# Performance work log

Hardware: AMD Instinct MI355X
Metric: run time of the kernel (lower is better)

Reference implementation:

```python
import jax, jax.numpy as jnp
import numpy as np

N = 100000   # nodes
E = 800000   # edges
H = 64       # hidden_channels (also input feature dim via lazy Linear)
OUT = 2      # out_channels
G = 64       # graphs in batch
EPS = 1e-5   # BatchNorm eps
N_PRE, N_CONV, N_POST = 3, 6, 3


def setup_inputs() -> dict:
    key = jax.random.key(0)
    ks = jax.random.split(key, 20)
    s = 0.1
    inp = {
        "x": jax.random.normal(ks[0], (N, H), jnp.float32),
        "edge_index": jax.random.randint(ks[1], (2, E), 0, N, dtype=jnp.int64),
        "batch": jnp.sort(jax.random.randint(ks[2], (N,), 0, G, dtype=jnp.int64)),
        # pre-processing MLP + BN params
        "pre_W": jax.random.normal(ks[3], (N_PRE, H, H), jnp.float32) * s,
        "pre_b": jax.random.normal(ks[4], (N_PRE, H), jnp.float32) * s,
        "pre_g": jnp.ones((N_PRE, H), jnp.float32),
        "pre_beta": jnp.zeros((N_PRE, H), jnp.float32),
        # GCNConv params (weight + bias per layer)
        "conv_W": jax.random.normal(ks[5], (N_CONV, H, H), jnp.float32) * s,
        "conv_b": jax.random.normal(ks[6], (N_CONV, H), jnp.float32) * s,
        # post-processing MLP + BN params
        "post_W": jax.random.normal(ks[7], (N_POST, H, H), jnp.float32) * s,
        "post_b": jax.random.normal(ks[8], (N_POST, H), jnp.float32) * s,
        "post_g": jnp.ones((N_POST, H), jnp.float32),
        "post_beta": jnp.zeros((N_POST, H), jnp.float32),
        # final head: H->H, H->H, H->OUT
        "fin_W0": jax.random.normal(ks[9], (H, H), jnp.float32) * s,
        "fin_b0": jax.random.normal(ks[10], (H,), jnp.float32) * s,
        "fin_W1": jax.random.normal(ks[11], (H, H), jnp.float32) * s,
        "fin_b1": jax.random.normal(ks[12], (H,), jnp.float32) * s,
        "fin_W2": jax.random.normal(ks[13], (H, OUT), jnp.float32) * s,
        "fin_b2": jax.random.normal(ks[14], (OUT,), jnp.float32) * s,
    }
    return inp


def _bn(h, g, b):
    # BatchNorm1d, training mode: biased batch statistics over node dim
    m = h.mean(0)
    v = h.var(0)
    return (h - m) * jax.lax.rsqrt(v + EPS) * g + b


def _gcn(h, src, dst, dinv, W, b):
    # PyG GCNConv: h' = D^-1/2 (A+I) D^-1/2 (h W) + b, sum-aggregated at dst
    hw = h @ W                                   # [N,H]
    norm = dinv[src] * dinv[dst]                 # [E]
    agg = jax.ops.segment_sum(hw[src] * norm[:, None], dst, num_segments=N)
    agg = agg + hw * (dinv * dinv)[:, None]      # self-loop contribution
    return agg + b


def reference(x, edge_index, batch, pre_W, pre_b, pre_g, pre_beta,
              conv_W, conv_b, post_W, post_b, post_g, post_beta,
              fin_W0, fin_b0, fin_W1, fin_b1, fin_W2, fin_b2):
    src, dst = edge_index[0], edge_index[1]
    # gcn_norm degree with self-loops (in-degree at dst), edge_weight = 1
    deg = jax.ops.segment_sum(jnp.ones((E,), x.dtype), dst, num_segments=N) + 1.0
    dinv = jax.lax.rsqrt(deg)

    h = x
    # pre-processing: Linear -> BN, relu except last
    for i in range(N_PRE):
        h = _bn(h @ pre_W[i] + pre_b[i], pre_g[i], pre_beta[i])
        if i != N_PRE - 1:
            h = jax.nn.relu(h)
    # GCNConv stack with residual adds
    for i in range(N_CONV):
        h = _gcn(h, src, dst, dinv, conv_W[i], conv_b[i]) + h
        if i != N_CONV - 1:
            h = jax.nn.relu(h)
    # post-processing: Linear -> BN, relu except last
    for i in range(N_POST):
        h = _bn(h @ post_W[i] + post_b[i], post_g[i], post_beta[i])
        if i != N_POST - 1:
            h = jax.nn.relu(h)
    # global_mean_pool over graphs
    counts = jax.ops.segment_sum(jnp.ones((N,), h.dtype), batch, num_segments=G)
    pooled = jax.ops.segment_sum(h, batch, num_segments=G) / jnp.maximum(counts, 1.0)[:, None]
    # final head (dropout is identity in eval)
    z = jax.nn.relu(pooled @ fin_W0 + fin_b0)
    z = jax.nn.relu(z @ fin_W1 + fin_b1)
    return z @ fin_W2 + fin_b2
```

## Files before the change

kernel.cpp:

```cpp
#include <hip/hip_runtime.h>

#define N_NODES 100000
#define N_EDGES 800000
#define HID 64
#define NGRAPH 64
#define OUTC 2
#define BN_EPS 1e-5f
#define GEMM_BLK ((N_NODES + 63) / 64)
#define POOL_SUB 16
#define BSHIFT 11
#define NBUCK 64
#define NBUCK_ACT ((N_NODES + (1 << BSHIFT) - 1) >> BSHIFT)
#define NEB_BLK ((N_EDGES + 2047) / 2048)

typedef __attribute__((ext_vector_type(8))) short bf16x8;
typedef __attribute__((ext_vector_type(4))) float f32x4;
typedef __attribute__((ext_vector_type(2))) float f32x2;

__device__ __forceinline__ unsigned short f2bf(float f) {
    unsigned int u = __float_as_uint(f);
    u = (u + 0x7FFFu + ((u >> 16) & 1u)) >> 16;
    return (unsigned short)u;
}
__device__ __forceinline__ float bflo(unsigned int u) { return __uint_as_float(u << 16); }
__device__ __forceinline__ float bfhi(unsigned int u) { return __uint_as_float(u & 0xFFFF0000u); }
__device__ __forceinline__ unsigned int bfpack(float a, float b) {
    return (unsigned int)f2bf(a) | ((unsigned int)f2bf(b) << 16);
}
__device__ __forceinline__ f32x2 bfpair(unsigned int w) {
    f32x2 p;
    p.x = __uint_as_float(w << 16);
    p.y = __uint_as_float(w & 0xFFFF0000u);
    return p;
}
__device__ __forceinline__ f32x2 pk_add(f32x2 a, f32x2 b) {
    f32x2 d;
    asm("v_pk_add_f32 %0, %1, %2" : "=v"(d) : "v"(a), "v"(b));
    return d;
}

template <int IN_MODE, bool IN_FP32, bool ADD_BIAS, bool ROW_SCALE, bool STATS>
__global__ __launch_bounds__(256) void k_gemm(const void* __restrict__ Xv,
                                              const float* __restrict__ W,
                                              const float* __restrict__ bias,
                                              const float* __restrict__ dinv,
                                              const float* __restrict__ scsh,
                                              unsigned short* __restrict__ Y,
                                              float* __restrict__ partial, int n) {
    __shared__ __align__(16) unsigned short sXb[64][72];
    __shared__ __align__(16) unsigned short sWT[64][72];
    __shared__ float sDinv[64];
    const int tid  = threadIdx.x;
    const int row0 = blockIdx.x * 64;

    #pragma unroll
    for (int i = tid; i < 1024; i += 256) {
        int k = i >> 4, c4 = (i & 15) << 2;
        float4 w = *reinterpret_cast<const float4*>(&W[k * 64 + c4]);
        sWT[c4 + 0][k] = f2bf(w.x);
        sWT[c4 + 1][k] = f2bf(w.y);
        sWT[c4 + 2][k] = f2bf(w.z);
        sWT[c4 + 3][k] = f2bf(w.w);
    }
    if (IN_FP32) {
        const float* X = (const float*)Xv;
        #pragma unroll
        for (int f = tid; f < 1024; f += 256) {
            int r = f >> 4, c4 = (f & 15) << 2;
            float4 v = make_float4(0.f, 0.f, 0.f, 0.f);
            if (row0 + r < n)
                v = *reinterpret_cast<const float4*>(&X[(size_t)(row0 + r) * HID + c4]);
            if (IN_MODE >= 1) {
                float4 sc = *reinterpret_cast<const float4*>(&scsh[c4]);
                float4 sh = *reinterpret_cast<const float4*>(&scsh[64 + c4]);
                v.x = v.x * sc.x + sh.x; v.y = v.y * sc.y + sh.y;
                v.z = v.z * sc.z + sh.z; v.w = v.w * sc.w + sh.w;
                if (IN_MODE == 2) {
                    v.x = fmaxf(v.x, 0.f); v.y = fmaxf(v.y, 0.f);
                    v.z = fmaxf(v.z, 0.f); v.w = fmaxf(v.w, 0.f);
                }
            }
            sXb[r][c4 + 0] = f2bf(v.x);
            sXb[r][c4 + 1] = f2bf(v.y);
            sXb[r][c4 + 2] = f2bf(v.z);
            sXb[r][c4 + 3] = f2bf(v.w);
        }
    } else {
        const unsigned short* X = (const unsigned short*)Xv;
        #pragma unroll
        for (int f = tid; f < 512; f += 256) {
            int r = f >> 3, c8 = (f & 7) << 3;
            uint4 u = make_uint4(0u, 0u, 0u, 0u);
            if (row0 + r < n)
                u = *reinterpret_cast<const uint4*>(&X[(size_t)(row0 + r) * HID + c8]);
            if (IN_MODE >= 1) {
                float v[8];
                v[0] = bflo(u.x); v[1] = bfhi(u.x);
                v[2] = bflo(u.y); v[3] = bfhi(u.y);
                v[4] = bflo(u.z); v[5] = bfhi(u.z);
                v[6] = bflo(u.w); v[7] = bfhi(u.w);
                #pragma unroll
                for (int k = 0; k < 8; ++k) {
                    v[k] = v[k] * scsh[c8 + k] + scsh[64 + c8 + k];
                    if (IN_MODE == 2) v[k] = fmaxf(v[k], 0.f);
                }
                u.x = bfpack(v[0], v[1]); u.y = bfpack(v[2], v[3]);
                u.z = bfpack(v[4], v[5]); u.w = bfpack(v[6], v[7]);
            }
            *reinterpret_cast<uint4*>(&sXb[r][c8]) = u;
        }
    }
    if (ROW_SCALE && tid < 64)
        sDinv[tid] = (row0 + tid < n) ? dinv[row0 + tid] : 0.f;
    __syncthreads();

    const int lane = tid & 63;
    const int wv   = tid >> 6;
    const int cl   = lane & 15;
    const int kg   = lane >> 4;
    const int col  = (wv << 4) + cl;

    const f32x4 zero = {0.f, 0.f, 0.f, 0.f};
    f32x4 acc[4];
    #pragma unroll
    for (int m = 0; m < 4; ++m) acc[m] = zero;

    #pragma unroll
    for (int k0 = 0; k0 < 64; k0 += 32) {
        bf16x8 bfrag = *reinterpret_cast<const bf16x8*>(&sWT[col][k0 + (kg << 3)]);
        #pragma unroll
        for (int m = 0; m < 4; ++m) {
            bf16x8 afrag = *reinterpret_cast<const bf16x8*>(&sXb[(m << 4) + cl][k0 + (kg << 3)]);
            acc[m] = __builtin_amdgcn_mfma_f32_16x16x32_bf16(afrag, bfrag, acc[m], 0, 0, 0);
        }
    }

    const float bb = ADD_BIAS ? bias[col] : 0.f;
    float colS = 0.f, colQ = 0.f;
    #pragma unroll
    for (int m = 0; m < 4; ++m) {
        #pragma unroll
        for (int j = 0; j < 4; ++j) {
            int rl = (m << 4) + (kg << 2) + j;
            int r  = row0 + rl;
            if (r < n) {
                float s = ROW_SCALE ? sDinv[rl] : 1.f;
                float o = acc[m][j] * s + bb;
                Y[(size_t)r * HID + col] = f2bf(o);
                if (STATS) { colS += o; colQ += o * o; }
            }
        }
    }
    if (STATS) {
        colS += __shfl_xor(colS, 16); colQ += __shfl_xor(colQ, 16);
        colS += __shfl_xor(colS, 32); colQ += __shfl_xor(colQ, 32);
        if (kg == 0) {
            partial[blockIdx.x * 128 + col]      = colS;
            partial[blockIdx.x * 128 + 64 + col] = colQ;
        }
    }
}

__global__ __launch_bounds__(256) void k_statsfin(const float* __restrict__ partial,
                                                  const float* __restrict__ g,
                                                  const float* __restrict__ beta,
                                                  float* __restrict__ scsh, int n) {
    int c = blockIdx.x, t = threadIdx.x;
    float S = 0.f, Q = 0.f;
    for (int b = t; b < GEMM_BLK; b += 256) {
        S += partial[b * 128 + c];
        Q += partial[b * 128 + 64 + c];
    }
    __shared__ float ss[256], sq[256];
    ss[t] = S; sq[t] = Q;
    __syncthreads();
    for (int off = 128; off > 0; off >>= 1) {
        if (t < off) { ss[t] += ss[t + off]; sq[t] += sq[t + off]; }
        __syncthreads();
    }
    if (t == 0) {
        float nf = (float)n;
        float m  = ss[0] / nf;
        float v  = sq[0] / nf - m * m;
        float sc = rsqrtf(v + BN_EPS) * g[c];
        scsh[c]      = sc;
        scsh[64 + c] = beta[c] - m * sc;
    }
}

__global__ __launch_bounds__(256) void k_hist(const int* __restrict__ dst,
                                              int* __restrict__ histmat) {
    __shared__ int lh[NBUCK];
    int t = threadIdx.x;
    if (t < NBUCK) lh[t] = 0;
    __syncthreads();
    int base = blockIdx.x * 2048;
    for (int i = t; i < 2048; i += 256) {
        int e = base + i;
        if (e < N_EDGES) atomicAdd(&lh[dst[e] >> BSHIFT], 1);
    }
    __syncthreads();
    if (t < NBUCK) histmat[blockIdx.x * NBUCK + t] = lh[t];
}

__global__ __launch_bounds__(256) void k_escan(const int* __restrict__ histmat,
                                               int* __restrict__ blockoff,
                                               int* __restrict__ bucketbase) {
    __shared__ int csum[4][NBUCK];
    __shared__ int cbase[4][NBUCK];
    __shared__ int tot[NBUCK + 1];
    int t = threadIdx.x;
    int b = t & 63, c = t >> 6;
    const int CHUNK = (NEB_BLK + 3) / 4;
    int lo = c * CHUNK, hi = min(lo + CHUNK, NEB_BLK);
    int s = 0;
    #pragma unroll 8
    for (int blk = lo; blk < hi; ++blk) s += histmat[blk * NBUCK + b];
    csum[c][b] = s;
    __syncthreads();
    if (t < NBUCK) {
        int r = 0;
        #pragma unroll
        for (int c2 = 0; c2 < 4; ++c2) { cbase[c2][t] = r; r += csum[c2][t]; }
        tot[t] = r;
    }
    __syncthreads();
    if (t == 0) {
        int r = 0;
        for (int b2 = 0; b2 < NBUCK; ++b2) { int v = tot[b2]; tot[b2] = r; r += v; }
        tot[NBUCK] = r;
    }
    __syncthreads();
    if (t <= NBUCK) bucketbase[t] = tot[t];
    int r = cbase[c][b];
    #pragma unroll 8
    for (int blk = lo; blk < hi; ++blk) {
        blockoff[blk * NBUCK + b] = r;
        r += histmat[blk * NBUCK + b];
    }
}

__global__ __launch_bounds__(256) void k_reorder(const int* __restrict__ src,
                                                 const int* __restrict__ dst,
                                                 const int* __restrict__ blockoff,
                                                 const int* __restrict__ bucketbase,
                                                 int2* __restrict__ esort) {
    __shared__ int lcur[NBUCK];
    int t = threadIdx.x;
    if (t < NBUCK) lcur[t] = 0;
    __syncthreads();
    int base = blockIdx.x * 2048;
    for (int i = t; i < 2048; i += 256) {
        int e = base + i;
        if (e < N_EDGES) {
            int d = dst[e];
            int b = d >> BSHIFT;
            int r = atomicAdd(&lcur[b], 1);
            esort[bucketbase[b] + blockoff[blockIdx.x * NBUCK + b] + r] =
                make_int2(src[e], d);
        }
    }
}

__global__ __launch_bounds__(256) void k_csr(const int2* __restrict__ esort,
                                             const int* __restrict__ bucketbase,
                                             int* __restrict__ rowptr,
                                             int* __restrict__ colidx,
                                             float* __restrict__ dinv,
                                             float* __restrict__ rdinv) {
    __shared__ int lh[1 << BSHIFT];
    __shared__ int ctot[256];
    int t = threadIdx.x;
    int b = blockIdx.x;
    int node0 = b << BSHIFT;
    int nNodes = min(1 << BSHIFT, N_NODES - node0);
    int e0 = bucketbase[b], e1 = bucketbase[b + 1];
    #pragma unroll
    for (int i = t; i < (1 << BSHIFT); i += 256) lh[i] = 0;
    __syncthreads();
    for (int e = e0 + t; e < e1; e += 256)
        atomicAdd(&lh[esort[e].y - node0], 1);
    __syncthreads();
    int c0 = t * 8;
    int cnt[8];
    int s = 0;
    #pragma unroll
    for (int j = 0; j < 8; ++j) { cnt[j] = lh[c0 + j]; s += cnt[j]; }
    ctot[t] = s;
    __syncthreads();
    int v = ctot[t];
    for (int off = 1; off < 256; off <<= 1) {
        int x = (t >= off) ? ctot[t - off] : 0;
        __syncthreads();
        ctot[t] += x;
        __syncthreads();
    }
    int run = ctot[t] - v;
    #pragma unroll
    for (int j = 0; j < 8; ++j) {
        int idx = c0 + j;
        int cv = cnt[j];
        lh[idx] = run;
        if (idx < nNodes) {
            rowptr[node0 + idx] = e0 + run;
            float dg = (float)cv + 1.f;
            dinv[node0 + idx]  = rsqrtf(dg);
            rdinv[node0 + idx] = sqrtf(dg);
        }
        run += cv;
    }
    __syncthreads();
    for (int e = e0 + t; e < e1; e += 256) {
        int2 ed = esort[e];
        int r = atomicAdd(&lh[ed.y - node0], 1);
        colidx[e0 + r] = ed.x;
    }
    if (b == 0 && t == 0) rowptr[N_NODES] = N_EDGES;
}

__global__ __launch_bounds__(256) void k_mkg(const unsigned short* __restrict__ H,
                                             const float* __restrict__ scsh,
                                             const float* __restrict__ dinv,
                                             unsigned short* __restrict__ G) {
    int i = blockIdx.x * 256 + threadIdx.x;
    if (i >= N_NODES * 8) return;
    int row = i >> 3, c8 = (i & 7) << 3;
    uint4 u = *reinterpret_cast<const uint4*>(&H[(size_t)row * HID + c8]);
    float di = dinv[row];
    float v[8];
    v[0] = bflo(u.x); v[1] = bfhi(u.x);
    v[2] = bflo(u.y); v[3] = bfhi(u.y);
    v[4] = bflo(u.z); v[5] = bfhi(u.z);
    v[6] = bflo(u.w); v[7] = bfhi(u.w);
    #pragma unroll
    for (int k = 0; k < 8; ++k)
        v[k] = (v[k] * scsh[c8 + k] + scsh[64 + c8 + k]) * di;
    uint4 o;
    o.x = bfpack(v[0], v[1]); o.y = bfpack(v[2], v[3]);
    o.z = bfpack(v[4], v[5]); o.w = bfpack(v[6], v[7]);
    *reinterpret_cast<uint4*>(&G[(size_t)row * HID + c8]) = o;
}

template <bool LAST>
__global__ __launch_bounds__(1024) void k_conv(const int* __restrict__ rowptr,
                                               const int* __restrict__ colidx,
                                               const unsigned short* __restrict__ G,
                                               const float* __restrict__ dinv,
                                               const float* __restrict__ rdinv,
                                               const float* __restrict__ W,
                                               const float* __restrict__ bias,
                                               unsigned short* __restrict__ OutT) {
    __shared__ __align__(16) unsigned short sXb[64][72];
    __shared__ __align__(16) unsigned short sG[64][72];
    __shared__ __align__(16) unsigned short sWT[64][72];
    __shared__ float red[16][8][64];
    __shared__ float sDinv[64], sRD[64];
    const int tid   = threadIdx.x;
    const int node0 = blockIdx.x * 64;

    {
        int k = tid >> 4, c4 = (tid & 15) << 2;
        float4 w = *reinterpret_cast<const float4*>(&W[k * 64 + c4]);
        sWT[c4 + 0][k] = f2bf(w.x);
        sWT[c4 + 1][k] = f2bf(w.y);
        sWT[c4 + 2][k] = f2bf(w.z);
        sWT[c4 + 3][k] = f2bf(w.w);
    }
    if (tid < 64) {
        int nd = node0 + tid;
        sDinv[tid] = (nd < N_NODES) ? dinv[nd] : 0.f;
        sRD[tid]   = (nd < N_NODES) ? rdinv[nd] : 0.f;
    }

    const int wv   = tid >> 6;
    const int lane = tid & 63;
    const int slot = lane >> 3;
    const int c8   = (lane & 7) << 3;

    #pragma unroll 1
    for (int it = 0; it < 4; ++it) {
        const int dl = (wv << 2) + it;
        const int d  = node0 + dl;
        const bool valid = d < N_NODES;

        f32x2 a0 = {0.f, 0.f}, a1 = {0.f, 0.f}, a2 = {0.f, 0.f}, a3 = {0.f, 0.f};
        if (valid) {
            if (slot == 7) {
                uint4 v = *reinterpret_cast<const uint4*>(&G[(size_t)d * HID + c8]);
                a0 = pk_add(a0, bfpair(v.x));
                a1 = pk_add(a1, bfpair(v.y));
                a2 = pk_add(a2, bfpair(v.z));
                a3 = pk_add(a3, bfpair(v.w));
            }
            const int j0 = rowptr[d], j1 = rowptr[d + 1];
            for (int j = j0 + slot; j < j1; j += 8) {
                int s = colidx[j];
                uint4 v = *reinterpret_cast<const uint4*>(&G[(size_t)s * HID + c8]);
                a0 = pk_add(a0, bfpair(v.x));
                a1 = pk_add(a1, bfpair(v.y));
                a2 = pk_add(a2, bfpair(v.z));
                a3 = pk_add(a3, bfpair(v.w));
            }
        }
        *reinterpret_cast<float4*>(&red[wv][slot][c8])     = make_float4(a0.x, a0.y, a1.x, a1.y);
        *reinterpret_cast<float4*>(&red[wv][slot][c8 + 4]) = make_float4(a2.x, a2.y, a3.x, a3.y);
        __builtin_amdgcn_wave_barrier();
        float s = 0.f;
        #pragma unroll
        for (int t2 = 0; t2 < 8; ++t2) s += red[wv][t2][lane];

        if (valid) {
            float z = s * sDinv[dl];
            sXb[dl][lane] = f2bf(z);
            sG[dl][lane]  = G[(size_t)d * HID + lane];
        } else {
            sXb[dl][lane] = 0;
            sG[dl][lane]  = 0;
        }
    }
    __syncthreads();

    const int rt = wv & 3, ct = wv >> 2;
    const int cl = lane & 15, kg = lane >> 4;
    const int col = (ct << 4) + cl;

    f32x4 acc = {0.f, 0.f, 0.f, 0.f};
    #pragma unroll
    for (int k0 = 0; k0 < 64; k0 += 32) {
        bf16x8 bfrag = *reinterpret_cast<const bf16x8*>(&sWT[col][k0 + (kg << 3)]);
        bf16x8 afrag = *reinterpret_cast<const bf16x8*>(&sXb[(rt << 4) + cl][k0 + (kg << 3)]);
        acc = __builtin_amdgcn_mfma_f32_16x16x32_bf16(afrag, bfrag, acc, 0, 0, 0);
    }

    const float bb = bias[col];
    #pragma unroll
    for (int j = 0; j < 4; ++j) {
        int rl = (rt << 4) + (kg << 2) + j;
        int r  = node0 + rl;
        if (r < N_NODES) {
            float h = bflo((unsigned int)sG[rl][col]) * sRD[rl];
            float o = acc[j] + bb + h;
            if (!LAST) {
                o = fmaxf(o, 0.f);
                o *= sDinv[rl];
            }
            OutT[(size_t)r * HID + col] = f2bf(o);
        }
    }
}

__device__ __forceinline__ int lowerb(const int* __restrict__ b, int n, int v) {
    int lo = 0, hi = n;
    while (lo < hi) { int m = (lo + hi) >> 1; if (b[m] < v) lo = m + 1; else hi = m; }
    return lo;
}

__global__ __launch_bounds__(256) void k_pool1(const unsigned short* __restrict__ Y,
                                               const int* __restrict__ batch,
                                               float* __restrict__ partial2) {
    int g  = blockIdx.x >> 4;
    int sb = blockIdx.x & 15;
    int tid = threadIdx.x, col = tid & 63, rg = tid >> 6;
    int lo = lowerb(batch, N_NODES, g);
    int hi = lowerb(batch, N_NODES, g + 1);
    int cnt = hi - lo;
    int st = lo + (int)(((long long)cnt * sb) >> 4);
    int en = lo + (int)(((long long)cnt * (sb + 1)) >> 4);
    float s = 0.f;
    for (int r = st + rg; r < en; r += 4)
        s += bflo((unsigned int)Y[(size_t)r * HID + col]);
    __shared__ float ls[4][64];
    ls[rg][col] = s;
    __syncthreads();
    if (tid < 64)
        partial2[(size_t)blockIdx.x * 64 + tid] =
            ls[0][tid] + ls[1][tid] + ls[2][tid] + ls[3][tid];
}

__global__ __launch_bounds__(256) void k_final(const float* __restrict__ partial2,
                                               const int* __restrict__ batch,
                                               const float* __restrict__ scsh,
                                               const float* __restrict__ W0,
                                               const float* __restrict__ b0,
                                               const float* __restrict__ W1,
                                               const float* __restrict__ b1,
                                               const float* __restrict__ W2,
                                               const float* __restrict__ b2,
                                               float* __restrict__ out) {
    __shared__ float sA[64][68];
    __shared__ float sC[64][68];
    __shared__ float sW[64][64];
    __shared__ int sOff[NGRAPH + 1];
    const int tid = threadIdx.x;
    const int tr = tid >> 4, tc = tid & 15;

    if (tid <= NGRAPH) sOff[tid] = lowerb(batch, N_NODES, tid);
    {
        const float4* w = reinterpret_cast<const float4*>(W0);
        float4* s = reinterpret_cast<float4*>(&sW[0][0]);
        #pragma unroll
        for (int i = tid; i < 1024; i += 256) s[i] = w[i];
    }
    __syncthreads();

    for (int i = tid; i < NGRAPH * HID; i += 256) {
        int g = i >> 6, c = i & 63;
        float S = 0.f;
        #pragma unroll
        for (int sb = 0; sb < POOL_SUB; ++sb)
            S += partial2[(size_t)(g * POOL_SUB + sb) * 64 + c];
        int cnt = sOff[g + 1] - sOff[g];
        float v = 0.f;
        if (cnt > 0) v = (S / (float)cnt) * scsh[c] + scsh[64 + c];
        sA[g][c] = v;
    }
    __syncthreads();

    {
        float4 acc[4];
        #pragma unroll
        for (int i = 0; i < 4; ++i) acc[i] = make_float4(0.f, 0.f, 0.f, 0.f);
        #pragma unroll 16
        for (int k = 0; k < 64; ++k) {
            const float4 bv = *reinterpret_cast<const float4*>(&sW[k][tc << 2]);
            float a[4];
            #pragma unroll
            for (int i = 0; i < 4; ++i) a[i] = sA[(tr << 2) + i][k];
            #pragma unroll
            for (int i = 0; i < 4; ++i) {
                acc[i].x += a[i] * bv.x; acc[i].y += a[i] * bv.y;
                acc[i].z += a[i] * bv.z; acc[i].w += a[i] * bv.w;
            }
        }
        float4 bb = *reinterpret_cast<const float4*>(&b0[tc << 2]);
        #pragma unroll
        for (int i = 0; i < 4; ++i) {
            float4 o;
            o.x = fmaxf(acc[i].x + bb.x, 0.f);
            o.y = fmaxf(acc[i].y + bb.y, 0.f);
            o.z = fmaxf(acc[i].z + bb.z, 0.f);
            o.w = fmaxf(acc[i].w + bb.w, 0.f);
            *reinterpret_cast<float4*>(&sC[(tr << 2) + i][tc << 2]) = o;
        }
    }
    __syncthreads();
    {
        const float4* w = reinterpret_cast<const float4*>(W1);
        float4* s = reinterpret_cast<float4*>(&sW[0][0]);
        #pragma unroll
        for (int i = tid; i < 1024; i += 256) s[i] = w[i];
    }
    __syncthreads();
    {
        float4 acc[4];
        #pragma unroll
        for (int i = 0; i < 4; ++i) acc[i] = make_float4(0.f, 0.f, 0.f, 0.f);
        #pragma unroll 16
        for (int k = 0; k < 64; ++k) {
            const float4 bv = *reinterpret_cast<const float4*>(&sW[k][tc << 2]);
            float a[4];
            #pragma unroll
            for (int i = 0; i < 4; ++i) a[i] = sC[(tr << 2) + i][k];
            #pragma unroll
            for (int i = 0; i < 4; ++i) {
                acc[i].x += a[i] * bv.x; acc[i].y += a[i] * bv.y;
                acc[i].z += a[i] * bv.z; acc[i].w += a[i] * bv.w;
            }
        }
        float4 bb = *reinterpret_cast<const float4*>(&b1[tc << 2]);
        #pragma unroll
        for (int i = 0; i < 4; ++i) {
            float4 o;
            o.x = fmaxf(acc[i].x + bb.x, 0.f);
            o.y = fmaxf(acc[i].y + bb.y, 0.f);
            o.z = fmaxf(acc[i].z + bb.z, 0.f);
            o.w = fmaxf(acc[i].w + bb.w, 0.f);
            *reinterpret_cast<float4*>(&sA[(tr << 2) + i][tc << 2]) = o;
        }
    }
    __syncthreads();

    if (tid < NGRAPH * OUTC) {
        int r = tid >> 1, c = tid & 1;
        float acc = b2[c];
        #pragma unroll 8
        for (int k = 0; k < 64; ++k) acc += sA[r][k] * W2[k * OUTC + c];
        out[tid] = acc;
    }
}

extern "C" void kernel_launch(void* const* d_in, const int* in_sizes, int n_in,
                              void* d_out, int out_size, void* d_ws, size_t ws_size,
                              hipStream_t stream) {
    const float* x        = (const float*)d_in[0];
    const int*   ei       = (const int*)d_in[1];
    const int*   batch    = (const int*)d_in[2];
    const float* pre_W    = (const float*)d_in[3];
    const float* pre_b    = (const float*)d_in[4];
    const float* pre_g    = (const float*)d_in[5];
    const float* pre_beta = (const float*)d_in[6];
    const float* conv_W   = (const float*)d_in[7];
    const float* conv_b   = (const float*)d_in[8];
    const float* post_W   = (const float*)d_in[9];
    const float* post_b   = (const float*)d_in[10];
    const float* post_g   = (const float*)d_in[11];
    const float* post_beta= (const float*)d_in[12];
    const float* fW0 = (const float*)d_in[13];
    const float* fb0 = (const float*)d_in[14];
    const float* fW1 = (const float*)d_in[15];
    const float* fb1 = (const float*)d_in[16];
    const float* fW2 = (const float*)d_in[17];
    const float* fb2 = (const float*)d_in[18];
    float* out = (float*)d_out;

    const size_t NH = (size_t)N_NODES * HID;
    unsigned short* Ab = (unsigned short*)d_ws;
    unsigned short* Bb = Ab + NH;
    unsigned short* Cb = Bb + NH;
    float* dinv     = (float*)(Cb + NH);
    float* rdinv    = dinv + N_NODES;
    float* partial  = rdinv + N_NODES;
    float* scsh     = partial + (size_t)GEMM_BLK*128;
    float* partial2 = scsh + 6 * 128;
    int* histmat    = (int*)(partial2 + NGRAPH * POOL_SUB * 64);
    int* blockoff   = histmat + NEB_BLK * NBUCK;
    int* bucketbase = blockoff + NEB_BLK * NBUCK;
    int* rowptr     = bucketbase + NBUCK + 1;
    int* colidx     = rowptr + N_NODES + 1;
    size_t eoff = (size_t)(colidx + N_EDGES - (int*)d_ws);
    eoff = (eoff + 1) & ~(size_t)1;
    int2* esort     = (int2*)((int*)d_ws + eoff);

    const int* srcp = ei;
    const int* dstp = ei + N_EDGES;

    k_hist<<<NEB_BLK, 256, 0, stream>>>(dstp, histmat);
    k_escan<<<1, 256, 0, stream>>>(histmat, blockoff, bucketbase);
    k_reorder<<<NEB_BLK, 256, 0, stream>>>(srcp, dstp, blockoff, bucketbase, esort);
    k_csr<<<NBUCK_ACT, 256, 0, stream>>>(esort, bucketbase, rowptr, colidx, dinv, rdinv);

    k_gemm<0, true,  true, false, true><<<GEMM_BLK, 256, 0, stream>>>(x, pre_W, pre_b, nullptr, nullptr, Ab, partial, N_NODES);
    k_statsfin<<<64, 256, 0, stream>>>(partial, pre_g, pre_beta, scsh + 0 * 128, N_NODES);

    k_gemm<2, false, true, false, true><<<GEMM_BLK, 256, 0, stream>>>(Ab, pre_W + 4096, pre_b + 64, nullptr, scsh + 0 * 128, Cb, partial, N_NODES);
    k_statsfin<<<64, 256, 0, stream>>>(partial, pre_g + 64, pre_beta + 64, scsh + 1 * 128, N_NODES);

    k_gemm<2, false, true, false, true><<<GEMM_BLK, 256, 0, stream>>>(Cb, pre_W + 2 * 4096, pre_b + 128, nullptr, scsh + 1 * 128, Ab, partial, N_NODES);
    k_statsfin<<<64, 256, 0, stream>>>(partial, pre_g + 128, pre_beta + 128, scsh + 2 * 128, N_NODES);

    k_mkg<<<(N_NODES * 8 + 255) / 256, 256, 0, stream>>>(Ab, scsh + 2 * 128, dinv, Bb);

    k_conv<false><<<GEMM_BLK, 1024, 0, stream>>>(rowptr, colidx, Bb, dinv, rdinv, conv_W + 0 * 4096, conv_b + 0 * 64, Cb);
    k_conv<false><<<GEMM_BLK, 1024, 0, stream>>>(rowptr, colidx, Cb, dinv, rdinv, conv_W + 1 * 4096, conv_b + 1 * 64, Bb);
    k_conv<false><<<GEMM_BLK, 1024, 0, stream>>>(rowptr, colidx, Bb, dinv, rdinv, conv_W + 2 * 4096, conv_b + 2 * 64, Cb);
    k_conv<false><<<GEMM_BLK, 1024, 0, stream>>>(rowptr, colidx, Cb, dinv, rdinv, conv_W + 3 * 4096, conv_b + 3 * 64, Bb);
    k_conv<false><<<GEMM_BLK, 1024, 0, stream>>>(rowptr, colidx, Bb, dinv, rdinv, conv_W + 4 * 4096, conv_b + 4 * 64, Cb);
    k_conv<true ><<<GEMM_BLK, 1024, 0, stream>>>(rowptr, colidx, Cb, dinv, rdinv, conv_W + 5 * 4096, conv_b + 5 * 64, Ab);

    k_gemm<0, false, true, false, true><<<GEMM_BLK, 256, 0, stream>>>(Ab, post_W, post_b, nullptr, nullptr, Cb, partial, N_NODES);
    k_statsfin<<<64, 256, 0, stream>>>(partial, post_g, post_beta, scsh + 3 * 128, N_NODES);

    k_gemm<2, false, true, false, true><<<GEMM_BLK, 256, 0, stream>>>(Cb, post_W + 4096, post_b + 64, nullptr, scsh + 3 * 128, Ab, partial, N_NODES);
    k_statsfin<<<64, 256, 0, stream>>>(partial, post_g + 64, post_beta + 64, scsh + 4 * 128, N_NODES);

    k_gemm<2, false, true, false, true><<<GEMM_BLK, 256, 0, stream>>>(Ab, post_W + 2 * 4096, post_b + 128, nullptr, scsh + 4 * 128, Cb, partial, N_NODES);
    k_statsfin<<<64, 256, 0, stream>>>(partial, post_g + 128, post_beta + 128, scsh + 5 * 128, N_NODES);

    k_pool1<<<NGRAPH * POOL_SUB, 256, 0, stream>>>(Cb, batch, partial2);
    k_final<<<1, 256, 0, stream>>>(partial2, batch, scsh + 5 * 128,
                                   fW0, fb0, fW1, fb1, fW2, fb2, out);
}
```

Measured before the change: 480.1 us.

## Shrink conv block tile to 16 nodes, one node per wave

The fused GCN conv kernel now handles 16 destination nodes per 1024-thread block instead of 64. Each wave aggregates exactly one node rather than looping over four, and only four waves run the MFMA transform. The grid grows fourfold, which should improve load balance and latency hiding for the irregular gather. The cost is that the bf16 transpose of the 64x64 weight into shared memory is repeated four times as often, and 12 of 16 waves sit idle during the GEMM. The reduction buffer is padded to 68 floats to avoid bank conflicts, and the bounds checks are dropped because N divides evenly by 16.

```diff
diff --git a/kernel.cpp b/kernel.cpp
--- a/kernel.cpp
+++ b/kernel.cpp
@@ -7,6 +7,7 @@
 #define OUTC 2
 #define BN_EPS 1e-5f
 #define GEMM_BLK ((N_NODES + 63) / 64)
+#define CONV_BLK (N_NODES / 16)
 #define POOL_SUB 16
 #define BSHIFT 11
 #define NBUCK 64
@@ -350,13 +351,13 @@
                                                const float* __restrict__ W,
                                                const float* __restrict__ bias,
                                                unsigned short* __restrict__ OutT) {
-    __shared__ __align__(16) unsigned short sXb[64][72];
-    __shared__ __align__(16) unsigned short sG[64][72];
+    __shared__ __align__(16) unsigned short sXb[16][72];
+    __shared__ __align__(16) unsigned short sG[16][72];
     __shared__ __align__(16) unsigned short sWT[64][72];
-    __shared__ float red[16][8][64];
-    __shared__ float sDinv[64], sRD[64];
+    __shared__ float red[16][8][68];
+    __shared__ float sDinv[16], sRD[16];
     const int tid   = threadIdx.x;
-    const int node0 = blockIdx.x * 64;
+    const int node0 = blockIdx.x * 16;
 
     {
         int k = tid >> 4, c4 = (tid & 15) << 2;
@@ -366,85 +367,66 @@
         sWT[c4 + 2][k] = f2bf(w.z);
         sWT[c4 + 3][k] = f2bf(w.w);
     }
-    if (tid < 64) {
-        int nd = node0 + tid;
-        sDinv[tid] = (nd < N_NODES) ? dinv[nd] : 0.f;
-        sRD[tid]   = (nd < N_NODES) ? rdinv[nd] : 0.f;
+    if (tid < 16) {
+        sDinv[tid] = dinv[node0 + tid];
+        sRD[tid]   = rdinv[node0 + tid];
     }
 
     const int wv   = tid >> 6;
     const int lane = tid & 63;
     const int slot = lane >> 3;
     const int c8   = (lane & 7) << 3;
-
-    #pragma unroll 1
-    for (int it = 0; it < 4; ++it) {
-        const int dl = (wv << 2) + it;
-        const int d  = node0 + dl;
-        const bool valid = d < N_NODES;
-
-        f32x2 a0 = {0.f, 0.f}, a1 = {0.f, 0.f}, a2 = {0.f, 0.f}, a3 = {0.f, 0.f};
-        if (valid) {
-            if (slot == 7) {
-                uint4 v = *reinterpret_cast<const uint4*>(&G[(size_t)d * HID + c8]);
-                a0 = pk_add(a0, bfpair(v.x));
-                a1 = pk_add(a1, bfpair(v.y));
-                a2 = pk_add(a2, bfpair(v.z));
-                a3 = pk_add(a3, bfpair(v.w));
-            }
-            const int j0 = rowptr[d], j1 = rowptr[d + 1];
-            for (int j = j0 + slot; j < j1; j += 8) {
-                int s = colidx[j];
-                uint4 v = *reinterpret_cast<const uint4*>(&G[(size_t)s * HID + c8]);
-                a0 = pk_add(a0, bfpair(v.x));
-                a1 = pk_add(a1, bfpair(v.y));
-                a2 = pk_add(a2, bfpair(v.z));
-                a3 = pk_add(a3, bfpair(v.w));
-            }
-        }
-        *reinterpret_cast<float4*>(&red[wv][slot][c8])     = make_float4(a0.x, a0.y, a1.x, a1.y);
-        *reinterpret_cast<float4*>(&red[wv][slot][c8 + 4]) = make_float4(a2.x, a2.y, a3.x, a3.y);
-        __builtin_amdgcn_wave_barrier();
-        float s = 0.f;
-        #pragma unroll
-        for (int t2 = 0; t2 < 8; ++t2) s += red[wv][t2][lane];
-
-        if (valid) {
-            float z = s * sDinv[dl];
-            sXb[dl][lane] = f2bf(z);
-            sG[dl][lane]  = G[(size_t)d * HID + lane];
-        } else {
-            sXb[dl][lane] = 0;
-            sG[dl][lane]  = 0;
-        }
-    }
-    __syncthreads();
-
-    const int rt = wv & 3, ct = wv >> 2;
-    const int cl = lane & 15, kg = lane >> 4;
-    const int col = (ct << 4) + cl;
-
-    f32x4 acc = {0.f, 0.f, 0.f, 0.f};
-    #pragma unroll
-    for (int k0 = 0; k0 < 64; k0 += 32) {
-        bf16x8 bfrag = *reinterpret_cast<const bf16x8*>(&sWT[col][k0 + (kg << 3)]);
-        bf16x8 afrag = *reinterpret_cast<const bf16x8*>(&sXb[(rt << 4) + cl][k0 + (kg << 3)]);
-        acc = __builtin_amdgcn_mfma_f32_16x16x32_bf16(afrag, bfrag, acc, 0, 0, 0);
-    }
-
-    const float bb = bias[col];
-    #pragma unroll
-    for (int j = 0; j < 4; ++j) {
-        int rl = (rt << 4) + (kg << 2) + j;
-        int r  = node0 + rl;
-        if (r < N_NODES) {
+    const int d    = node0 + wv;
+
+    f32x2 a0 = {0.f, 0.f}, a1 = {0.f, 0.f}, a2 = {0.f, 0.f}, a3 = {0.f, 0.f};
+    if (slot == 7) {
+        uint4 v = *reinterpret_cast<const uint4*>(&G[(size_t)d * HID + c8]);
+        a0 = pk_add(a0, bfpair(v.x));
+        a1 = pk_add(a1, bfpair(v.y));
+        a2 = pk_add(a2, bfpair(v.z));
+        a3 = pk_add(a3, bfpair(v.w));
+    }
+    for (int j = rowptr[d] + slot, e = rowptr[d + 1]; j < e; j += 8) {
+        int s = colidx[j];
+        uint4 v = *reinterpret_cast<const uint4*>(&G[(size_t)s * HID + c8]);
+        a0 = pk_add(a0, bfpair(v.x));
+        a1 = pk_add(a1, bfpair(v.y));
+        a2 = pk_add(a2, bfpair(v.z));
+        a3 = pk_add(a3, bfpair(v.w));
+    }
+
+    *reinterpret_cast<float4*>(&red[wv][slot][c8])     = make_float4(a0.x, a0.y, a1.x, a1.y);
+    *reinterpret_cast<float4*>(&red[wv][slot][c8 + 4]) = make_float4(a2.x, a2.y, a3.x, a3.y);
+    __builtin_amdgcn_wave_barrier();
+    float s = 0.f;
+    #pragma unroll
+    for (int t2 = 0; t2 < 8; ++t2) s += red[wv][t2][lane];
+
+    sXb[wv][lane] = f2bf(s * sDinv[wv]);
+    sG[wv][lane]  = G[(size_t)d * HID + lane];
+    __syncthreads();
+
+    if (wv < 4) {
+        const int cl = lane & 15, kg = lane >> 4;
+        const int col = (wv << 4) + cl;
+        f32x4 acc = {0.f, 0.f, 0.f, 0.f};
+        #pragma unroll
+        for (int k0 = 0; k0 < 64; k0 += 32) {
+            bf16x8 bfrag = *reinterpret_cast<const bf16x8*>(&sWT[col][k0 + (kg << 3)]);
+            bf16x8 afrag = *reinterpret_cast<const bf16x8*>(&sXb[cl][k0 + (kg << 3)]);
+            acc = __builtin_amdgcn_mfma_f32_16x16x32_bf16(afrag, bfrag, acc, 0, 0, 0);
+        }
+        const float bb = bias[col];
+        #pragma unroll
+        for (int j = 0; j < 4; ++j) {
+            int rl = (kg << 2) + j;
             float h = bflo((unsigned int)sG[rl][col]) * sRD[rl];
             float o = acc[j] + bb + h;
             if (!LAST) {
                 o = fmaxf(o, 0.f);
                 o *= sDinv[rl];
             }
-            OutT[(size_t)r * HID + col] = f2bf(o);
+            OutT[(size_t)(node0 + rl) * HID + col] = f2bf(o);
         }
     }
 }
@@ -650,12 +632,12 @@
 
     k_mkg<<<(N_NODES * 8 + 255) / 256, 256, 0, stream>>>(Ab, scsh + 2 * 128, dinv, Bb);
 
-    k_conv<false><<<GEMM_BLK, 1024, 0, stream>>>(rowptr, colidx, Bb, dinv, rdinv, conv_W + 0 * 4096, conv_b + 0 * 64, Cb);
-    k_conv<false><<<GEMM_BLK, 1024, 0, stream>>>(rowptr, colidx, Cb, dinv, rdinv, conv_W + 1 * 4096, conv_b + 1 * 64, Bb);
-    k_conv<false><<<GEMM_BLK, 1024, 0, stream>>>(rowptr, colidx, Bb, dinv, rdinv, conv_W + 2 * 4096, conv_b + 2 * 64, Cb);
-    k_conv<false><<<GEMM_BLK, 1024, 0, stream>>>(rowptr, colidx, Cb, dinv, rdinv, conv_W + 3 * 4096, conv_b + 3 * 64, Bb);
-    k_conv<false><<<GEMM_BLK, 1024, 0, stream>>>(rowptr, colidx, Bb, dinv, rdinv, conv_W + 4 * 4096, conv_b + 4 * 64, Cb);
-    k_conv<true ><<<GEMM_BLK, 1024, 0, stream>>>(rowptr, colidx, Cb, dinv, rdinv, conv_W + 5 * 4096, conv_b + 5 * 64, Ab);
+    k_conv<false><<<CONV_BLK, 1024, 0, stream>>>(rowptr, colidx, Bb, dinv, rdinv, conv_W + 0 * 4096, conv_b + 0 * 64, Cb);
+    k_conv<false><<<CONV_BLK, 1024, 0, stream>>>(rowptr, colidx, Cb, dinv, rdinv, conv_W + 1 * 4096, conv_b + 1 * 64, Bb);
+    k_conv<false><<<CONV_BLK, 1024, 0, stream>>>(rowptr, colidx, Bb, dinv, rdinv, conv_W + 2 * 4096, conv_b + 2 * 64, Cb);
+    k_conv<false><<<CONV_BLK, 1024, 0, stream>>>(rowptr, colidx, Cb, dinv, rdinv, conv_W + 3 * 4096, conv_b + 3 * 64, Bb);
+    k_conv<false><<<CONV_BLK, 1024, 0, stream>>>(rowptr, colidx, Bb, dinv, rdinv, conv_W + 4 * 4096, conv_b + 4 * 64, Cb);
+    k_conv<true ><<<CONV_BLK, 1024, 0, stream>>>(rowptr, colidx, Cb, dinv, rdinv, conv_W + 5 * 4096, conv_b + 5 * 64, Ab);
 
     k_gemm<0, false, true, false, true><<<GEMM_BLK, 256, 0, stream>>>(Ab, post_W, post_b, nullptr, nullptr, Cb, partial, N_NODES);
     k_statsfin<<<64, 256, 0, stream>>>(partial, post_g, post_beta, scsh + 3 * 128, N_NODES);
```

Result: slower. 499.2 us (+4.0%).
